# Performance work log

Measured on AMD Instinct MI355X. Metric: run time of the kernel, lower is better.

## Reference

```python
import jax, jax.numpy as jnp
import numpy as np

D_MODEL = 1024
D_STATE = 16
D_CONV = 4
EXPAND = 2
D_INNER = EXPAND * D_MODEL           # 2048
DT_RANK = (D_MODEL + 15) // 16       # 64
BATCH = 2
SEQ = 1024


def setup_inputs() -> dict:
    key = jax.random.key(0)
    ks = jax.random.split(key, 8)
    s = 0.02
    x = jax.random.normal(ks[0], (BATCH, SEQ, D_MODEL), jnp.float32)
    in_proj_w = jax.random.normal(ks[1], (2 * D_INNER, D_MODEL), jnp.float32) * s
    conv_w = jax.random.normal(ks[2], (D_INNER, 1, D_CONV), jnp.float32) * s
    conv_b = jnp.zeros((D_INNER,), jnp.float32)
    x_proj_w = jax.random.normal(ks[3], (DT_RANK + 2 * D_STATE, D_INNER), jnp.float32) * s
    dt_proj_w = jax.random.normal(ks[4], (D_INNER, DT_RANK), jnp.float32) * s
    # bias init so softplus(dt) lands in a sane small-dt range
    dt_proj_b = jnp.full((D_INNER,), -4.0, jnp.float32) + 0.1 * jax.random.normal(ks[5], (D_INNER,), jnp.float32)
    # standard S4D-real init: A = -[1..d_state], stored as log
    A_log = jnp.log(jnp.broadcast_to(jnp.arange(1, D_STATE + 1, dtype=jnp.float32), (D_INNER, D_STATE)))
    D_param = jnp.ones((D_INNER,), jnp.float32)
    out_proj_w = jax.random.normal(ks[6], (D_MODEL, D_INNER), jnp.float32) * s
    ln_w = jnp.ones((D_MODEL,), jnp.float32)
    ln_b = jnp.zeros((D_MODEL,), jnp.float32)
    return dict(x=x, in_proj_w=in_proj_w, conv_w=conv_w, conv_b=conv_b,
                x_proj_w=x_proj_w, dt_proj_w=dt_proj_w, dt_proj_b=dt_proj_b,
                A_log=A_log, D_param=D_param, out_proj_w=out_proj_w,
                ln_w=ln_w, ln_b=ln_b)


def _vim_block(x, in_proj_w, conv_w, conv_b, x_proj_w, dt_proj_w, dt_proj_b,
               A_log, D_param, out_proj_w, ln_w, ln_b):
    B, L, Dm = x.shape
    # in_proj (no bias) -> split into conv branch and gate z
    xz = jnp.einsum('bld,ed->ble', x, in_proj_w)          # (B,L,2*d_inner)
    xc, z = jnp.split(xz, 2, axis=-1)
    # causal depthwise conv1d over time
    xc_ncl = jnp.transpose(xc, (0, 2, 1))                  # (B,d_inner,L)
    conv = jax.lax.conv_general_dilated(
        xc_ncl, conv_w, window_strides=(1,), padding=[(D_CONV - 1, 0)],
        dimension_numbers=('NCH', 'OIH', 'NCH'), feature_group_count=D_INNER)
    conv = conv + conv_b[None, :, None]
    u = jax.nn.silu(jnp.transpose(conv, (0, 2, 1)))        # (B,L,d_inner)
    # input-dependent dt, B, C
    x_dbl = jnp.einsum('bld,ed->ble', u, x_proj_w)         # (B,L,dt_rank+2N)
    dt, Bmat, Cmat = jnp.split(x_dbl, [DT_RANK, DT_RANK + D_STATE], axis=-1)
    delta = jax.nn.softplus(jnp.einsum('blr,dr->bld', dt, dt_proj_w) + dt_proj_b)  # (B,L,d_inner)
    A = -jnp.exp(A_log)                                    # (d_inner,N)
    # discretize: ZOH for A, Euler for B (as in mamba selective_scan)
    deltaA = jnp.exp(delta[..., None] * A)                 # (B,L,d_inner,N)
    deltaBu = (delta * u)[..., None] * Bmat[:, :, None, :] # (B,L,d_inner,N)

    def step(h, inp):
        dA_t, dBu_t, C_t = inp                             # (B,d,N),(B,d,N),(B,N)
        h = dA_t * h + dBu_t
        y_t = jnp.einsum('bdn,bn->bd', h, C_t)
        return h, y_t

    h0 = jnp.zeros((B, D_INNER, D_STATE), x.dtype)
    xs = (jnp.moveaxis(deltaA, 1, 0), jnp.moveaxis(deltaBu, 1, 0), jnp.moveaxis(Cmat, 1, 0))
    _, ys = jax.lax.scan(step, h0, xs)                     # ys: (L,B,d_inner)
    y = jnp.moveaxis(ys, 0, 1) + u * D_param               # (B,L,d_inner)
    y = y * jax.nn.silu(z)                                 # gate
    out = jnp.einsum('bld,ed->ble', y, out_proj_w)         # (B,L,D)
    # residual + LayerNorm
    r = x + out
    mu = jnp.mean(r, axis=-1, keepdims=True)
    var = jnp.mean(jnp.square(r - mu), axis=-1, keepdims=True)
    return (r - mu) * jax.lax.rsqrt(var + 1e-5) * ln_w + ln_b


def reference(x, in_proj_w, conv_w, conv_b, x_proj_w, dt_proj_w, dt_proj_b,
              A_log, D_param, out_proj_w, ln_w, ln_b):
    return _vim_block(x, in_proj_w, conv_w, conv_b, x_proj_w, dt_proj_w, dt_proj_b,
                      A_log, D_param, out_proj_w, ln_w, ln_b)
```

## Files before the change

kernel.cpp:

```cpp
#include <hip/hip_runtime.h>
#include <math.h>

#define D_MODEL 1024
#define D_STATE 16
#define D_INNER 2048
#define DT_RANK 64
#define BATCH 2
#define SEQ 1024
#define NTOK (BATCH*SEQ)
#define NC 32
#define TC 32

typedef __attribute__((ext_vector_type(8))) short short8;
typedef __attribute__((ext_vector_type(4))) float f32x4;

__device__ __forceinline__ float siluf(float x){ return x / (1.0f + __expf(-x)); }
__device__ __forceinline__ float softplusf(float x){ return x > 20.f ? x : log1pf(__expf(x)); }

__device__ __forceinline__ unsigned short f2bf(float f){
    unsigned int x = __float_as_uint(f);
    unsigned int r = (x + 0x7FFFu + ((x >> 16) & 1u)) >> 16;
    return (unsigned short)r;
}
__device__ __forceinline__ float bf2f(unsigned short u){
    return __uint_as_float(((unsigned int)u) << 16);
}

__device__ __forceinline__ void gl_lds16(const unsigned short* g, unsigned short* l)
{
    __builtin_amdgcn_global_load_lds(
        (const __attribute__((address_space(1))) unsigned int*)g,
        (__attribute__((address_space(3))) unsigned int*)l, 16, 0, 0);
}

#define CR0 524288
#define CR1 1572864
#define CR2 1622016
#define CR3 1654784
#define CR4 2179072
__global__ __launch_bounds__(256)
void cvt_all(const float* __restrict__ s0, const float* __restrict__ s1,
             const float* __restrict__ s2, const float* __restrict__ s3,
             const float* __restrict__ s4,
             unsigned short* __restrict__ d0, unsigned short* __restrict__ d1,
             unsigned short* __restrict__ d2, unsigned short* __restrict__ d3,
             unsigned short* __restrict__ d4)
{
    int i = blockIdx.x * 256 + threadIdx.x;
    const float* s; unsigned short* dd; int base;
    if      (i < CR0) { s = s0; dd = d0; base = 0;   }
    else if (i < CR1) { s = s1; dd = d1; base = CR0; }
    else if (i < CR2) { s = s2; dd = d2; base = CR1; }
    else if (i < CR3) { s = s3; dd = d3; base = CR2; }
    else              { s = s4; dd = d4; base = CR3; }
    int j = (i - base) * 4;
    float4 v = *reinterpret_cast<const float4*>(&s[j]);
    ushort4 o;
    o.x = f2bf(v.x); o.y = f2bf(v.y); o.z = f2bf(v.z); o.w = f2bf(v.w);
    *reinterpret_cast<ushort4*>(&dd[j]) = o;
}

template<int EPI, int OB, int NVALID>
__global__ __launch_bounds__(256)
void gemm128(const unsigned short* __restrict__ A, int lda,
             const unsigned short* __restrict__ W, int ldw,
             const float* __restrict__ bias,
             void* __restrict__ Cv, int ldc,
             int M, int K)
{
    __shared__ __align__(16) unsigned short As[2][128 * 32];
    __shared__ __align__(16) unsigned short Ws[2][128 * 32];
    float* Cf = (float*)Cv;
    unsigned short* Cb = (unsigned short*)Cv;
    const int tid = threadIdx.x;

    const int nwg = gridDim.x * gridDim.y;
    int orig = blockIdx.y * gridDim.x + blockIdx.x;
    const int q = nwg >> 3, r = nwg & 7;
    int xcd = orig & 7, sub = orig >> 3;
    int wg = (xcd < r ? xcd * (q + 1) : r * (q + 1) + (xcd - r) * q) + sub;
    const int m0 = (wg / gridDim.x) * 128;
    const int n0 = (wg % gridDim.x) * 128;

    const size_t kbase = (size_t)blockIdx.z * K;
    const size_t zoff = (size_t)blockIdx.z * M * ldc;
    Cf += zoff; Cb += zoff;

    const int wave = tid >> 6, lane = tid & 63;
    const int wr = wave >> 1, wc = wave & 1;
    const int lr = lane & 15, lg = lane >> 4;

    const int gr = lane >> 2;
    const int gc = (lane & 3) * 8;
    const unsigned short* Ab = A + kbase + gc + (size_t)(m0 + wave * 32 + gr) * lda;
    const unsigned short* Wb = W + kbase + gc + (size_t)(n0 + wave * 32 + gr) * ldw;
    const int lo = (wave * 32) * 32;

    f32x4 acc[4][4];
#pragma unroll
    for (int i = 0; i < 4; i++)
#pragma unroll
        for (int j = 0; j < 4; j++) acc[i][j] = (f32x4)0.f;

    auto STAGE = [&](int buf, int kk) {
        gl_lds16(Ab + kk,            &As[buf][lo]);
        gl_lds16(Ab + kk + 16 * lda, &As[buf][lo + 16 * 32]);
        gl_lds16(Wb + kk,            &Ws[buf][lo]);
        gl_lds16(Wb + kk + 16 * ldw, &Ws[buf][lo + 16 * 32]);
    };
    auto COMPUTE = [&](int buf) {
        short8 af[4], bfr[4];
#pragma unroll
        for (int i = 0; i < 4; i++)
            af[i] = *reinterpret_cast<const short8*>(&As[buf][(wr * 64 + i * 16 + lr) * 32 + lg * 8]);
#pragma unroll
        for (int j = 0; j < 4; j++)
            bfr[j] = *reinterpret_cast<const short8*>(&Ws[buf][(wc * 64 + j * 16 + lr) * 32 + lg * 8]);
#pragma unroll
        for (int i = 0; i < 4; i++)
#pragma unroll
            for (int j = 0; j < 4; j++)
                acc[i][j] = __builtin_amdgcn_mfma_f32_16x16x32_bf16(af[i], bfr[j], acc[i][j], 0, 0, 0);
    };

    STAGE(0, 0);
    __syncthreads();
    for (int k0 = 0; k0 < K; k0 += 64) {
        if (k0 + 32 < K) STAGE(1, k0 + 32);
        COMPUTE(0);
        __syncthreads();
        if (k0 + 64 < K) STAGE(0, k0 + 64);
        COMPUTE(1);
        __syncthreads();
    }

#pragma unroll
    for (int i = 0; i < 4; i++) {
#pragma unroll
        for (int j = 0; j < 4; j++) {
            int col = n0 + wc * 64 + j * 16 + lr;
            if (NVALID > 0 && col >= NVALID) continue;
            int rbase = m0 + wr * 64 + i * 16 + lg * 4;
#pragma unroll
            for (int q2 = 0; q2 < 4; q2++) {
                float v = acc[i][j][q2];
                if (EPI == 1) v = softplusf(v + bias[col]);
                if (OB) Cb[(size_t)(rbase + q2) * ldc + col] = f2bf(v);
                else    Cf[(size_t)(rbase + q2) * ldc + col] = v;
            }
        }
    }
}

__global__ __launch_bounds__(256)
void conv_silu(const unsigned short* __restrict__ xz, const float* __restrict__ cw,
               const float* __restrict__ cb, unsigned short* __restrict__ u)
{
    int idx = blockIdx.x * 256 + threadIdx.x;
    int c = idx & (D_INNER - 1);
    int l = (idx >> 11) & (SEQ - 1);
    int b = idx >> 21;
    float4 w = *reinterpret_cast<const float4*>(&cw[c * 4]);
    float wk[4] = {w.x, w.y, w.z, w.w};
    float acc = cb[c];
    const unsigned short* xp = xz + (size_t)b * SEQ * (2 * D_INNER) + c;
#pragma unroll
    for (int k = 0; k < 4; k++) {
        int lk = l - 3 + k;
        if (lk >= 0) acc = fmaf(wk[k], bf2f(xp[(size_t)lk * (2 * D_INNER)]), acc);
    }
    u[idx] = f2bf(siluf(acc));
}

__global__ __launch_bounds__(256)
void reduce_xproj(const float* __restrict__ part, float* __restrict__ xdbl,
                  unsigned short* __restrict__ dt_bf)
{
    int idx = blockIdx.x * 256 + threadIdx.x;
    float s = 0.f;
#pragma unroll
    for (int z = 0; z < 8; z++) s += part[(size_t)z * NTOK * 96 + idx];
    xdbl[idx] = s;
    int c = idx % 96, m = idx / 96;
    if (c < DT_RANK) dt_bf[m * DT_RANK + c] = f2bf(s);
}

__global__ __launch_bounds__(256)
void scan_phase1(const unsigned short* __restrict__ delta, const unsigned short* __restrict__ u,
                 const float* __restrict__ xdbl,  const float* __restrict__ A_log,
                 float* __restrict__ P, float* __restrict__ Q)
{
    __shared__ float sB[TC][16];
    const int tid = threadIdx.x;
    const int dblk = blockIdx.x & 7;
    const int cc = (blockIdx.x >> 3) & (NC - 1);
    const int b  = blockIdx.x >> 8;
    const int d  = dblk * 256 + tid;
    const int t0 = cc * TC;

    float A[16];
#pragma unroll
    for (int i = 0; i < 4; i++) {
        float4 al = *reinterpret_cast<const float4*>(&A_log[d * 16 + i * 4]);
        A[i*4+0] = -__expf(al.x); A[i*4+1] = -__expf(al.y);
        A[i*4+2] = -__expf(al.z); A[i*4+3] = -__expf(al.w);
    }
    for (int e = tid; e < TC * 16; e += 256) {
        int t = e >> 4, j = e & 15;
        sB[t][j] = xdbl[((size_t)b * SEQ + t0 + t) * 96 + DT_RANK + j];
    }
    __syncthreads();

    float h[16];
#pragma unroll
    for (int n = 0; n < 16; n++) h[n] = 0.f;
    float sum = 0.f;
#pragma unroll 4
    for (int t = 0; t < TC; t++) {
        size_t tok = (size_t)b * SEQ + t0 + t;
        float dv = bf2f(delta[tok * D_INNER + d]);
        float uv = bf2f(u[tok * D_INNER + d]);
        sum += dv;
        float du = dv * uv;
#pragma unroll
        for (int n = 0; n < 16; n++)
            h[n] = fmaf(__expf(dv * A[n]), h[n], du * sB[t][n]);
    }
    size_t off = ((size_t)(cc * BATCH + b) * D_INNER + d) * 16;
#pragma unroll
    for (int i = 0; i < 4; i++) {
        float4 pv = make_float4(__expf(A[i*4+0]*sum), __expf(A[i*4+1]*sum),
                                __expf(A[i*4+2]*sum), __expf(A[i*4+3]*sum));
        *reinterpret_cast<float4*>(&P[off + i*4]) = pv;
        *reinterpret_cast<float4*>(&Q[off + i*4]) =
            make_float4(h[i*4+0], h[i*4+1], h[i*4+2], h[i*4+3]);
    }
}

__global__ __launch_bounds__(256)
void scan_phase2(const float* __restrict__ P, float* __restrict__ Q)
{
    int idx = blockIdx.x * 256 + threadIdx.x;
    int b = idx >> 15, rem = idx & 32767;
    float h = 0.f;
#pragma unroll
    for (int cc = 0; cc < NC; cc++) {
        size_t off = (size_t)(cc * BATCH + b) * (D_INNER * D_STATE) + rem;
        float p = P[off], q = Q[off];
        Q[off] = h;
        h = fmaf(p, h, q);
    }
}

__global__ __launch_bounds__(256)
void scan_phase3(const unsigned short* __restrict__ delta, const unsigned short* __restrict__ u,
                 const unsigned short* __restrict__ xz, const float* __restrict__ xdbl,
                 const float* __restrict__ A_log, const float* __restrict__ Dp,
                 const float* __restrict__ Hin,   unsigned short* __restrict__ yg)
{
    __shared__ float sB[TC][16], sC[TC][16];
    const int tid = threadIdx.x;
    const int dblk = blockIdx.x & 7;
    const int cc = (blockIdx.x >> 3) & (NC - 1);
    const int b  = blockIdx.x >> 8;
    const int d  = dblk * 256 + tid;
    const int t0 = cc * TC;

    float A[16];
#pragma unroll
    for (int i = 0; i < 4; i++) {
        float4 al = *reinterpret_cast<const float4*>(&A_log[d * 16 + i * 4]);
        A[i*4+0] = -__expf(al.x); A[i*4+1] = -__expf(al.y);
        A[i*4+2] = -__expf(al.z); A[i*4+3] = -__expf(al.w);
    }
    const float Dcoef = Dp[d];
    for (int e = tid; e < TC * 16; e += 256) {
        int t = e >> 4, j = e & 15;
        size_t tok = (size_t)b * SEQ + t0 + t;
        sB[t][j] = xdbl[tok * 96 + DT_RANK + j];
        sC[t][j] = xdbl[tok * 96 + DT_RANK + D_STATE + j];
    }
    float h[16];
    {
        size_t off = ((size_t)(cc * BATCH + b) * D_INNER + d) * 16;
#pragma unroll
        for (int i = 0; i < 4; i++) {
            float4 hv = *reinterpret_cast<const float4*>(&Hin[off + i*4]);
            h[i*4+0] = hv.x; h[i*4+1] = hv.y; h[i*4+2] = hv.z; h[i*4+3] = hv.w;
        }
    }
    __syncthreads();

#pragma unroll 4
    for (int t = 0; t < TC; t++) {
        size_t tok = (size_t)b * SEQ + t0 + t;
        float dv = bf2f(delta[tok * D_INNER + d]);
        float uv = bf2f(u[tok * D_INNER + d]);
        float zv = bf2f(xz[tok * (2 * D_INNER) + D_INNER + d]);
        float du = dv * uv;
        float y = 0.f;
#pragma unroll
        for (int n = 0; n < 16; n++) {
            h[n] = fmaf(__expf(dv * A[n]), h[n], du * sB[t][n]);
            y = fmaf(h[n], sC[t][n], y);
        }
        y += uv * Dcoef;
        yg[tok * D_INNER + d] = f2bf(y * siluf(zv));
    }
}

__global__ __launch_bounds__(256)
void ln4_kernel(const float* __restrict__ x, const unsigned short* __restrict__ p,
                const float* __restrict__ w, const float* __restrict__ bsc,
                float* __restrict__ out)
{
    __shared__ float red[2][4];
    const int t = blockIdx.x;
    const size_t base = (size_t)t * D_MODEL;
    const size_t S = (size_t)NTOK * D_MODEL;
    const int tid = threadIdx.x;
    const int c0 = tid * 4;
    float4 xv = *reinterpret_cast<const float4*>(&x[base + c0]);
    ushort4 p0 = *reinterpret_cast<const ushort4*>(&p[base + c0]);
    ushort4 p1 = *reinterpret_cast<const ushort4*>(&p[S + base + c0]);
    ushort4 p2 = *reinterpret_cast<const ushort4*>(&p[2 * S + base + c0]);
    ushort4 p3 = *reinterpret_cast<const ushort4*>(&p[3 * S + base + c0]);
    float v[4];
    v[0] = xv.x + bf2f(p0.x) + bf2f(p1.x) + bf2f(p2.x) + bf2f(p3.x);
    v[1] = xv.y + bf2f(p0.y) + bf2f(p1.y) + bf2f(p2.y) + bf2f(p3.y);
    v[2] = xv.z + bf2f(p0.z) + bf2f(p1.z) + bf2f(p2.z) + bf2f(p3.z);
    v[3] = xv.w + bf2f(p0.w) + bf2f(p1.w) + bf2f(p2.w) + bf2f(p3.w);
    float s = 0.f, s2 = 0.f;
#pragma unroll
    for (int i = 0; i < 4; i++) { s += v[i]; s2 = fmaf(v[i], v[i], s2); }
#pragma unroll
    for (int off = 32; off >= 1; off >>= 1) {
        s  += __shfl_down(s,  off);
        s2 += __shfl_down(s2, off);
    }
    int lane = tid & 63, wid = tid >> 6;
    if (lane == 0) { red[0][wid] = s; red[1][wid] = s2; }
    __syncthreads();
    float S1 = red[0][0] + red[0][1] + red[0][2] + red[0][3];
    float S2 = red[1][0] + red[1][1] + red[1][2] + red[1][3];
    float mu  = S1 * (1.f / D_MODEL);
    float var = S2 * (1.f / D_MODEL) - mu * mu;
    float rstd = rsqrtf(var + 1e-5f);
    float4 wv = *reinterpret_cast<const float4*>(&w[c0]);
    float4 bv = *reinterpret_cast<const float4*>(&bsc[c0]);
    float4 ov;
    ov.x = (v[0] - mu) * rstd * wv.x + bv.x;
    ov.y = (v[1] - mu) * rstd * wv.y + bv.y;
    ov.z = (v[2] - mu) * rstd * wv.z + bv.z;
    ov.w = (v[3] - mu) * rstd * wv.w + bv.w;
    *reinterpret_cast<float4*>(&out[base + c0]) = ov;
}

extern "C" void kernel_launch(void* const* d_in, const int* in_sizes, int n_in,
                              void* d_out, int out_size, void* d_ws, size_t ws_size,
                              hipStream_t stream)
{
    const float* x         = (const float*)d_in[0];
    const float* in_proj_w = (const float*)d_in[1];
    const float* conv_w    = (const float*)d_in[2];
    const float* conv_b    = (const float*)d_in[3];
    const float* x_proj_w  = (const float*)d_in[4];
    const float* dt_proj_w = (const float*)d_in[5];
    const float* dt_proj_b = (const float*)d_in[6];
    const float* A_log     = (const float*)d_in[7];
    const float* D_param   = (const float*)d_in[8];
    const float* out_proj_w= (const float*)d_in[9];
    const float* ln_w      = (const float*)d_in[10];
    const float* ln_b      = (const float*)d_in[11];
    float* out = (float*)d_out;

    unsigned short* xzb = (unsigned short*)d_ws;
    float* xdbl     = (float*)(xzb + (size_t)NTOK * 4096);
    float* partials = xdbl + (size_t)NTOK * 96;
    unsigned short* dlb = (unsigned short*)(partials + (size_t)8 * NTOK * 96);
    unsigned short* ub  = dlb + (size_t)NTOK * D_INNER;
    unsigned short* ygb = ub  + (size_t)NTOK * D_INNER;
    unsigned short* xb  = ygb + (size_t)NTOK * D_INNER;
    unsigned short* wib = xb  + (size_t)NTOK * D_MODEL;
    unsigned short* wxb = wib + (size_t)4096 * 1024;
    unsigned short* wdb = wxb + (size_t)96 * 2048;
    unsigned short* wob = wdb + (size_t)2048 * 64;
    unsigned short* dtb = wob + (size_t)1024 * 2048;
    float* Pbuf = (float*)(dtb + (size_t)NTOK * 64);
    float* Qbuf = Pbuf + (size_t)NC * BATCH * D_INNER * D_STATE;
    unsigned short* opart = xzb;

    dim3 blk(256);

    cvt_all<<<dim3(CR4 / 256), blk, 0, stream>>>(
        x, in_proj_w, x_proj_w, dt_proj_w, out_proj_w,
        xb, wib, wxb, wdb, wob);

    gemm128<0, 1, 0><<<dim3(4096 / 128, NTOK / 128, 1), blk, 0, stream>>>(
        xb, D_MODEL, wib, D_MODEL, nullptr, xzb, 2 * D_INNER, NTOK, D_MODEL);

    conv_silu<<<dim3((NTOK * D_INNER) / 256), blk, 0, stream>>>(xzb, conv_w, conv_b, ub);

    gemm128<0, 0, 96><<<dim3(1, NTOK / 128, 8), blk, 0, stream>>>(
        ub, D_INNER, wxb, D_INNER, nullptr, partials, 96, NTOK, 2048 / 8);

    reduce_xproj<<<dim3((NTOK * 96) / 256), blk, 0, stream>>>(partials, xdbl, dtb);

    gemm128<1, 1, 0><<<dim3(D_INNER / 128, NTOK / 128, 1), blk, 0, stream>>>(
        dtb, DT_RANK, wdb, DT_RANK, dt_proj_b, dlb, D_INNER, NTOK, DT_RANK);

    scan_phase1<<<dim3(BATCH * NC * (D_INNER / 256)), blk, 0, stream>>>(
        dlb, ub, xdbl, A_log, Pbuf, Qbuf);
    scan_phase2<<<dim3((BATCH * D_INNER * D_STATE) / 256), blk, 0, stream>>>(Pbuf, Qbuf);
    scan_phase3<<<dim3(BATCH * NC * (D_INNER / 256)), blk, 0, stream>>>(
        dlb, ub, xzb, xdbl, A_log, D_param, Qbuf, ygb);

    gemm128<0, 1, 0><<<dim3(D_MODEL / 128, NTOK / 128, 4), blk, 0, stream>>>(
        ygb, D_INNER, wob, D_INNER, nullptr, opart, D_MODEL, NTOK, D_INNER / 4);

    ln4_kernel<<<dim3(NTOK), blk, 0, stream>>>(x, opart, ln_w, ln_b, out);
}
```

Measured before the change: 173.1 us.

## Increase split-K across all GEMMs and vectorize conv with summed partials

The in_proj GEMM is split-K by 2, x_proj by 16 and out_proj by 8, so each launch has more blocks to fill the GPU. The conv and scan_phase3 consumers now sum the two in_proj bf16 partials on read, and the LayerNorm kernel sums eight out_proj partials. The conv kernel is vectorized to process four channels per thread, and the workspace layout is reshuffled to alias P/Q onto the x buffer. The cost is extra partial-buffer memory traffic and extra bf16 rounding error from summing partials.

Result: slower. 187.2 us (+8.2%).

```diff
diff --git a/kernel.cpp b/kernel.cpp
--- a/kernel.cpp
+++ b/kernel.cpp
@@ -153,23 +153,44 @@
 }
 
 __global__ __launch_bounds__(256)
-void conv_silu(const unsigned short* __restrict__ xz, const float* __restrict__ cw,
-               const float* __restrict__ cb, unsigned short* __restrict__ u)
-{
+void conv_silu4(const unsigned short* __restrict__ xzp, const float* __restrict__ cw,
+                const float* __restrict__ cb, unsigned short* __restrict__ u)
+{
+    const size_t PS = (size_t)NTOK * 4096;
     int idx = blockIdx.x * 256 + threadIdx.x;
-    int c = idx & (D_INNER - 1);
-    int l = (idx >> 11) & (SEQ - 1);
-    int b = idx >> 21;
-    float4 w = *reinterpret_cast<const float4*>(&cw[c * 4]);
-    float wk[4] = {w.x, w.y, w.z, w.w};
-    float acc = cb[c];
-    const unsigned short* xp = xz + (size_t)b * SEQ * (2 * D_INNER) + c;
+    int cq  = idx & 511;
+    int c0  = cq * 4;
+    int tok = idx >> 9;
+    int l   = tok & (SEQ - 1);
+
+    float4 w0 = *reinterpret_cast<const float4*>(&cw[(c0 + 0) * 4]);
+    float4 w1 = *reinterpret_cast<const float4*>(&cw[(c0 + 1) * 4]);
+    float4 w2 = *reinterpret_cast<const float4*>(&cw[(c0 + 2) * 4]);
+    float4 w3 = *reinterpret_cast<const float4*>(&cw[(c0 + 3) * 4]);
+    float4 bv = *reinterpret_cast<const float4*>(&cb[c0]);
+    float acc0 = bv.x, acc1 = bv.y, acc2 = bv.z, acc3 = bv.w;
+
 #pragma unroll
     for (int k = 0; k < 4; k++) {
         int lk = l - 3 + k;
-        if (lk >= 0) acc = fmaf(wk[k], bf2f(xp[(size_t)lk * (2 * D_INNER)]), acc);
-    }
-    u[idx] = f2bf(siluf(acc));
+        if (lk >= 0) {
+            size_t base = (size_t)(tok - 3 + k) * 4096 + c0;
+            ushort4 a = *reinterpret_cast<const ushort4*>(&xzp[base]);
+            ushort4 b = *reinterpret_cast<const ushort4*>(&xzp[PS + base]);
+            float x0 = bf2f(a.x) + bf2f(b.x);
+            float x1 = bf2f(a.y) + bf2f(b.y);
+            float x2 = bf2f(a.z) + bf2f(b.z);
+            float x3 = bf2f(a.w) + bf2f(b.w);
+            acc0 = fmaf(((const float*)&w0)[k], x0, acc0);
+            acc1 = fmaf(((const float*)&w1)[k], x1, acc1);
+            acc2 = fmaf(((const float*)&w2)[k], x2, acc2);
+            acc3 = fmaf(((const float*)&w3)[k], x3, acc3);
+        }
+    }
+    ushort4 o;
+    o.x = f2bf(siluf(acc0)); o.y = f2bf(siluf(acc1));
+    o.z = f2bf(siluf(acc2)); o.w = f2bf(siluf(acc3));
+    *reinterpret_cast<ushort4*>(&u[(size_t)tok * D_INNER + c0]) = o;
 }
 
 __global__ __launch_bounds__(256)
@@ -179,7 +200,7 @@
     int idx = blockIdx.x * 256 + threadIdx.x;
     float s = 0.f;
 #pragma unroll
-    for (int z = 0; z < 8; z++) s += part[(size_t)z * NTOK * 96 + idx];
+    for (int z = 0; z < 16; z++) s += part[(size_t)z * NTOK * 96 + idx];
     xdbl[idx] = s;
     int c = idx % 96, m = idx / 96;
     if (c < DT_RANK) dt_bf[m * DT_RANK + c] = f2bf(s);
@@ -254,11 +275,12 @@
 
 __global__ __launch_bounds__(256)
 void scan_phase3(const unsigned short* __restrict__ delta, const unsigned short* __restrict__ u,
-                 const unsigned short* __restrict__ xz, const float* __restrict__ xdbl,
+                 const unsigned short* __restrict__ xzp, const float* __restrict__ xdbl,
                  const float* __restrict__ A_log, const float* __restrict__ Dp,
                  const float* __restrict__ Hin,   unsigned short* __restrict__ yg)
 {
     __shared__ float sB[TC][16], sC[TC][16];
+    const size_t PS = (size_t)NTOK * 4096;
     const int tid = threadIdx.x;
     const int dblk = blockIdx.x & 7;
     const int cc = (blockIdx.x >> 3) & (NC - 1);
@@ -296,7 +318,8 @@
         size_t tok = (size_t)b * SEQ + t0 + t;
         float dv = bf2f(delta[tok * D_INNER + d]);
         float uv = bf2f(u[tok * D_INNER + d]);
-        float zv = bf2f(xz[tok * (2 * D_INNER) + D_INNER + d]);
+        size_t zi = tok * 4096 + D_INNER + d;
+        float zv = bf2f(xzp[zi]) + bf2f(xzp[PS + zi]);
         float du = dv * uv;
         float y = 0.f;
 #pragma unroll
@@ -310,7 +333,7 @@
 }
 
 __global__ __launch_bounds__(256)
-void ln4_kernel(const float* __restrict__ x, const unsigned short* __restrict__ p,
+void ln8_kernel(const float* __restrict__ x, const unsigned short* __restrict__ p,
                 const float* __restrict__ w, const float* __restrict__ bsc,
                 float* __restrict__ out)
 {
@@ -321,15 +344,13 @@
     const int tid = threadIdx.x;
     const int c0 = tid * 4;
     float4 xv = *reinterpret_cast<const float4*>(&x[base + c0]);
-    ushort4 p0 = *reinterpret_cast<const ushort4*>(&p[base + c0]);
-    ushort4 p1 = *reinterpret_cast<const ushort4*>(&p[S + base + c0]);
-    ushort4 p2 = *reinterpret_cast<const ushort4*>(&p[2 * S + base + c0]);
-    ushort4 p3 = *reinterpret_cast<const ushort4*>(&p[3 * S + base + c0]);
-    float v[4];
-    v[0] = xv.x + bf2f(p0.x) + bf2f(p1.x) + bf2f(p2.x) + bf2f(p3.x);
-    v[1] = xv.y + bf2f(p0.y) + bf2f(p1.y) + bf2f(p2.y) + bf2f(p3.y);
-    v[2] = xv.z + bf2f(p0.z) + bf2f(p1.z) + bf2f(p2.z) + bf2f(p3.z);
-    v[3] = xv.w + bf2f(p0.w) + bf2f(p1.w) + bf2f(p2.w) + bf2f(p3.w);
+    float v[4] = {xv.x, xv.y, xv.z, xv.w};
+#pragma unroll
+    for (int z = 0; z < 8; z++) {
+        ushort4 pv = *reinterpret_cast<const ushort4*>(&p[z * S + base + c0]);
+        v[0] += bf2f(pv.x); v[1] += bf2f(pv.y);
+        v[2] += bf2f(pv.z); v[3] += bf2f(pv.w);
+    }
     float s = 0.f, s2 = 0.f;
 #pragma unroll
     for (int i = 0; i < 4; i++) { s += v[i]; s2 = fmaf(v[i], v[i], s2); }
@@ -374,21 +395,21 @@
     const float* ln_b      = (const float*)d_in[11];
     float* out = (float*)d_out;
 
-    unsigned short* xzb = (unsigned short*)d_ws;
-    float* xdbl     = (float*)(xzb + (size_t)NTOK * 4096);
-    float* partials = xdbl + (size_t)NTOK * 96;
-    unsigned short* dlb = (unsigned short*)(partials + (size_t)8 * NTOK * 96);
+    unsigned short* xzp = (unsigned short*)d_ws;
+    float* xdbl = (float*)(xzp + (size_t)2 * NTOK * 4096);
+    unsigned short* dlb = (unsigned short*)(xdbl + (size_t)NTOK * 96);
     unsigned short* ub  = dlb + (size_t)NTOK * D_INNER;
     unsigned short* ygb = ub  + (size_t)NTOK * D_INNER;
     unsigned short* xb  = ygb + (size_t)NTOK * D_INNER;
     unsigned short* wib = xb  + (size_t)NTOK * D_MODEL;
     unsigned short* wxb = wib + (size_t)4096 * 1024;
     unsigned short* wdb = wxb + (size_t)96 * 2048;
-    unsigned short* wob = wdb + (size_t)2048 * 64;
-    unsigned short* dtb = wob + (size_t)1024 * 2048;
-    float* Pbuf = (float*)(dtb + (size_t)NTOK * 64);
+    unsigned short* dtb = wdb + (size_t)2048 * 64;
+    float* xpart = (float*)(dtb + (size_t)NTOK * 64);
+    float* Pbuf = (float*)xb;
     float* Qbuf = Pbuf + (size_t)NC * BATCH * D_INNER * D_STATE;
-    unsigned short* opart = xzb;
+    unsigned short* wob = (unsigned short*)(xpart + (size_t)16 * NTOK * 96);
+    unsigned short* opart = xzp;
 
     dim3 blk(256);
 
@@ -396,15 +417,15 @@
         x, in_proj_w, x_proj_w, dt_proj_w, out_proj_w,
         xb, wib, wxb, wdb, wob);
 
-    gemm128<0, 1, 0><<<dim3(4096 / 128, NTOK / 128, 1), blk, 0, stream>>>(
-        xb, D_MODEL, wib, D_MODEL, nullptr, xzb, 2 * D_INNER, NTOK, D_MODEL);
-
-    conv_silu<<<dim3((NTOK * D_INNER) / 256), blk, 0, stream>>>(xzb, conv_w, conv_b, ub);
-
-    gemm128<0, 0, 96><<<dim3(1, NTOK / 128, 8), blk, 0, stream>>>(
-        ub, D_INNER, wxb, D_INNER, nullptr, partials, 96, NTOK, 2048 / 8);
-
-    reduce_xproj<<<dim3((NTOK * 96) / 256), blk, 0, stream>>>(partials, xdbl, dtb);
+    gemm128<0, 1, 0><<<dim3(4096 / 128, NTOK / 128, 2), blk, 0, stream>>>(
+        xb, D_MODEL, wib, D_MODEL, nullptr, xzp, 2 * D_INNER, NTOK, D_MODEL / 2);
+
+    conv_silu4<<<dim3((NTOK * 512) / 256), blk, 0, stream>>>(xzp, conv_w, conv_b, ub);
+
+    gemm128<0, 0, 96><<<dim3(1, NTOK / 128, 16), blk, 0, stream>>>(
+        ub, D_INNER, wxb, D_INNER, nullptr, xpart, 96, NTOK, 2048 / 16);
+
+    reduce_xproj<<<dim3((NTOK * 96) / 256), blk, 0, stream>>>(xpart, xdbl, dtb);
 
     gemm128<1, 1, 0><<<dim3(D_INNER / 128, NTOK / 128, 1), blk, 0, stream>>>(
         dtb, DT_RANK, wdb, DT_RANK, dt_proj_b, dlb, D_INNER, NTOK, DT_RANK);
@@ -413,10 +434,10 @@
         dlb, ub, xdbl, A_log, Pbuf, Qbuf);
     scan_phase2<<<dim3((BATCH * D_INNER * D_STATE) / 256), blk, 0, stream>>>(Pbuf, Qbuf);
     scan_phase3<<<dim3(BATCH * NC * (D_INNER / 256)), blk, 0, stream>>>(
-        dlb, ub, xzb, xdbl, A_log, D_param, Qbuf, ygb);
-
-    gemm128<0, 1, 0><<<dim3(D_MODEL / 128, NTOK / 128, 4), blk, 0, stream>>>(
-        ygb, D_INNER, wob, D_INNER, nullptr, opart, D_MODEL, NTOK, D_INNER / 4);
-
-    ln4_kernel<<<dim3(NTOK), blk, 0, stream>>>(x, opart, ln_w, ln_b, out);
-}
+        dlb, ub, xzp, xdbl, A_log, D_param, Qbuf, ygb);
+
+    gemm128<0, 1, 0><<<dim3(D_MODEL / 128, NTOK / 128, 8), blk, 0, stream>>>(
+        ygb, D_INNER, wob, D_INNER, nullptr, opart, D_MODEL, NTOK, D_INNER / 8);
+
+    ln8_kernel<<<dim3(NTOK), blk, 0, stream>>>(x, opart, ln_w, ln_b, out);
+}
```

## Fuse three scan phases into one cooperative kernel and vectorize conv

Applied to the files above, without the earlier changes.

The three chunked-scan kernels become one cooperative kernel that uses grid-wide syncs between the chunk-local scan, the cross-chunk carry propagation and the output pass. This removes two kernel launches and their tail gaps. The depthwise conv kernel now handles four channels per thread with ushort4 loads and stores instead of one scalar element per thread. The cooperative launch requires all 512 blocks to be resident at once, and the grid syncs add barrier cost.

After: 326.0 us. 88.3% more time.

```diff
diff --git a/kernel.cpp b/kernel.cpp
--- a/kernel.cpp
+++ b/kernel.cpp
@@ -1,5 +1,8 @@
 #include <hip/hip_runtime.h>
+#include <hip/hip_cooperative_groups.h>
 #include <math.h>
+
+namespace cg = cooperative_groups;
 
 #define D_MODEL 1024
 #define D_STATE 16
@@ -153,23 +156,38 @@
 }
 
 __global__ __launch_bounds__(256)
-void conv_silu(const unsigned short* __restrict__ xz, const float* __restrict__ cw,
-               const float* __restrict__ cb, unsigned short* __restrict__ u)
+void conv_silu4(const unsigned short* __restrict__ xz, const float* __restrict__ cw,
+                const float* __restrict__ cb, unsigned short* __restrict__ u)
 {
     int idx = blockIdx.x * 256 + threadIdx.x;
-    int c = idx & (D_INNER - 1);
-    int l = (idx >> 11) & (SEQ - 1);
-    int b = idx >> 21;
-    float4 w = *reinterpret_cast<const float4*>(&cw[c * 4]);
-    float wk[4] = {w.x, w.y, w.z, w.w};
-    float acc = cb[c];
-    const unsigned short* xp = xz + (size_t)b * SEQ * (2 * D_INNER) + c;
+    int cq  = idx & 511;
+    int c0  = cq * 4;
+    int tok = idx >> 9;
+    int l   = tok & (SEQ - 1);
+
+    float4 w0 = *reinterpret_cast<const float4*>(&cw[(c0 + 0) * 4]);
+    float4 w1 = *reinterpret_cast<const float4*>(&cw[(c0 + 1) * 4]);
+    float4 w2 = *reinterpret_cast<const float4*>(&cw[(c0 + 2) * 4]);
+    float4 w3 = *reinterpret_cast<const float4*>(&cw[(c0 + 3) * 4]);
+    float4 bv = *reinterpret_cast<const float4*>(&cb[c0]);
+    float acc0 = bv.x, acc1 = bv.y, acc2 = bv.z, acc3 = bv.w;
+
 #pragma unroll
     for (int k = 0; k < 4; k++) {
         int lk = l - 3 + k;
-        if (lk >= 0) acc = fmaf(wk[k], bf2f(xp[(size_t)lk * (2 * D_INNER)]), acc);
-    }
-    u[idx] = f2bf(siluf(acc));
+        if (lk >= 0) {
+            size_t base = (size_t)(tok - 3 + k) * 4096 + c0;
+            ushort4 a = *reinterpret_cast<const ushort4*>(&xz[base]);
+            acc0 = fmaf(((const float*)&w0)[k], bf2f(a.x), acc0);
+            acc1 = fmaf(((const float*)&w1)[k], bf2f(a.y), acc1);
+            acc2 = fmaf(((const float*)&w2)[k], bf2f(a.z), acc2);
+            acc3 = fmaf(((const float*)&w3)[k], bf2f(a.w), acc3);
+        }
+    }
+    ushort4 o;
+    o.x = f2bf(siluf(acc0)); o.y = f2bf(siluf(acc1));
+    o.z = f2bf(siluf(acc2)); o.w = f2bf(siluf(acc3));
+    *reinterpret_cast<ushort4*>(&u[(size_t)tok * D_INNER + c0]) = o;
 }
 
 __global__ __launch_bounds__(256)
@@ -186,78 +204,13 @@
 }
 
 __global__ __launch_bounds__(256)
-void scan_phase1(const unsigned short* __restrict__ delta, const unsigned short* __restrict__ u,
-                 const float* __restrict__ xdbl,  const float* __restrict__ A_log,
-                 float* __restrict__ P, float* __restrict__ Q)
-{
-    __shared__ float sB[TC][16];
-    const int tid = threadIdx.x;
-    const int dblk = blockIdx.x & 7;
-    const int cc = (blockIdx.x >> 3) & (NC - 1);
-    const int b  = blockIdx.x >> 8;
-    const int d  = dblk * 256 + tid;
-    const int t0 = cc * TC;
-
-    float A[16];
-#pragma unroll
-    for (int i = 0; i < 4; i++) {
-        float4 al = *reinterpret_cast<const float4*>(&A_log[d * 16 + i * 4]);
-        A[i*4+0] = -__expf(al.x); A[i*4+1] = -__expf(al.y);
-        A[i*4+2] = -__expf(al.z); A[i*4+3] = -__expf(al.w);
-    }
-    for (int e = tid; e < TC * 16; e += 256) {
-        int t = e >> 4, j = e & 15;
-        sB[t][j] = xdbl[((size_t)b * SEQ + t0 + t) * 96 + DT_RANK + j];
-    }
-    __syncthreads();
-
-    float h[16];
-#pragma unroll
-    for (int n = 0; n < 16; n++) h[n] = 0.f;
-    float sum = 0.f;
-#pragma unroll 4
-    for (int t = 0; t < TC; t++) {
-        size_t tok = (size_t)b * SEQ + t0 + t;
-        float dv = bf2f(delta[tok * D_INNER + d]);
-        float uv = bf2f(u[tok * D_INNER + d]);
-        sum += dv;
-        float du = dv * uv;
-#pragma unroll
-        for (int n = 0; n < 16; n++)
-            h[n] = fmaf(__expf(dv * A[n]), h[n], du * sB[t][n]);
-    }
-    size_t off = ((size_t)(cc * BATCH + b) * D_INNER + d) * 16;
-#pragma unroll
-    for (int i = 0; i < 4; i++) {
-        float4 pv = make_float4(__expf(A[i*4+0]*sum), __expf(A[i*4+1]*sum),
-                                __expf(A[i*4+2]*sum), __expf(A[i*4+3]*sum));
-        *reinterpret_cast<float4*>(&P[off + i*4]) = pv;
-        *reinterpret_cast<float4*>(&Q[off + i*4]) =
-            make_float4(h[i*4+0], h[i*4+1], h[i*4+2], h[i*4+3]);
-    }
-}
-
-__global__ __launch_bounds__(256)
-void scan_phase2(const float* __restrict__ P, float* __restrict__ Q)
-{
-    int idx = blockIdx.x * 256 + threadIdx.x;
-    int b = idx >> 15, rem = idx & 32767;
-    float h = 0.f;
-#pragma unroll
-    for (int cc = 0; cc < NC; cc++) {
-        size_t off = (size_t)(cc * BATCH + b) * (D_INNER * D_STATE) + rem;
-        float p = P[off], q = Q[off];
-        Q[off] = h;
-        h = fmaf(p, h, q);
-    }
-}
-
-__global__ __launch_bounds__(256)
-void scan_phase3(const unsigned short* __restrict__ delta, const unsigned short* __restrict__ u,
-                 const unsigned short* __restrict__ xz, const float* __restrict__ xdbl,
-                 const float* __restrict__ A_log, const float* __restrict__ Dp,
-                 const float* __restrict__ Hin,   unsigned short* __restrict__ yg)
-{
+void scan_fused(const unsigned short* __restrict__ delta, const unsigned short* __restrict__ u,
+                const unsigned short* __restrict__ xz,    const float* __restrict__ xdbl,
+                const float* __restrict__ A_log, const float* __restrict__ Dp,
+                float* __restrict__ P, float* __restrict__ Q,
+                unsigned short* __restrict__ yg)
+{
+    cg::grid_group grid = cg::this_grid();
     __shared__ float sB[TC][16], sC[TC][16];
     const int tid = threadIdx.x;
     const int dblk = blockIdx.x & 7;
@@ -280,32 +233,76 @@
         sB[t][j] = xdbl[tok * 96 + DT_RANK + j];
         sC[t][j] = xdbl[tok * 96 + DT_RANK + D_STATE + j];
     }
-    float h[16];
+    __syncthreads();
+
+    const size_t off = ((size_t)(cc * BATCH + b) * D_INNER + d) * 16;
+
     {
-        size_t off = ((size_t)(cc * BATCH + b) * D_INNER + d) * 16;
+        float h[16];
+#pragma unroll
+        for (int n = 0; n < 16; n++) h[n] = 0.f;
+        float sum = 0.f;
+#pragma unroll 4
+        for (int t = 0; t < TC; t++) {
+            size_t tok = (size_t)b * SEQ + t0 + t;
+            float dv = bf2f(delta[tok * D_INNER + d]);
+            float uv = bf2f(u[tok * D_INNER + d]);
+            sum += dv;
+            float du = dv * uv;
+#pragma unroll
+            for (int n = 0; n < 16; n++)
+                h[n] = fmaf(__expf(dv * A[n]), h[n], du * sB[t][n]);
+        }
 #pragma unroll
         for (int i = 0; i < 4; i++) {
-            float4 hv = *reinterpret_cast<const float4*>(&Hin[off + i*4]);
+            float4 pv = make_float4(__expf(A[i*4+0]*sum), __expf(A[i*4+1]*sum),
+                                    __expf(A[i*4+2]*sum), __expf(A[i*4+3]*sum));
+            *reinterpret_cast<float4*>(&P[off + i*4]) = pv;
+            *reinterpret_cast<float4*>(&Q[off + i*4]) =
+                make_float4(h[i*4+0], h[i*4+1], h[i*4+2], h[i*4+3]);
+        }
+    }
+    grid.sync();
+
+    {
+        int idx = blockIdx.x * 256 + tid;
+        if (idx < BATCH * D_INNER * D_STATE) {
+            int bb = idx >> 15, rem = idx & 32767;
+            float h = 0.f;
+#pragma unroll
+            for (int c2 = 0; c2 < NC; c2++) {
+                size_t o2 = (size_t)(c2 * BATCH + bb) * (D_INNER * D_STATE) + rem;
+                float p = P[o2], qv = Q[o2];
+                Q[o2] = h;
+                h = fmaf(p, h, qv);
+            }
+        }
+    }
+    grid.sync();
+
+    {
+        float h[16];
+#pragma unroll
+        for (int i = 0; i < 4; i++) {
+            float4 hv = *reinterpret_cast<const float4*>(&Q[off + i*4]);
             h[i*4+0] = hv.x; h[i*4+1] = hv.y; h[i*4+2] = hv.z; h[i*4+3] = hv.w;
         }
-    }
-    __syncthreads();
-
 #pragma unroll 4
-    for (int t = 0; t < TC; t++) {
-        size_t tok = (size_t)b * SEQ + t0 + t;
-        float dv = bf2f(delta[tok * D_INNER + d]);
-        float uv = bf2f(u[tok * D_INNER + d]);
-        float zv = bf2f(xz[tok * (2 * D_INNER) + D_INNER + d]);
-        float du = dv * uv;
-        float y = 0.f;
-#pragma unroll
-        for (int n = 0; n < 16; n++) {
-            h[n] = fmaf(__expf(dv * A[n]), h[n], du * sB[t][n]);
-            y = fmaf(h[n], sC[t][n], y);
-        }
-        y += uv * Dcoef;
-        yg[tok * D_INNER + d] = f2bf(y * siluf(zv));
+        for (int t = 0; t < TC; t++) {
+            size_t tok = (size_t)b * SEQ + t0 + t;
+            float dv = bf2f(delta[tok * D_INNER + d]);
+            float uv = bf2f(u[tok * D_INNER + d]);
+            float zv = bf2f(xz[tok * (2 * D_INNER) + D_INNER + d]);
+            float du = dv * uv;
+            float y = 0.f;
+#pragma unroll
+            for (int n = 0; n < 16; n++) {
+                h[n] = fmaf(__expf(dv * A[n]), h[n], du * sB[t][n]);
+                y = fmaf(h[n], sC[t][n], y);
+            }
+            y += uv * Dcoef;
+            yg[tok * D_INNER + d] = f2bf(y * siluf(zv));
+        }
     }
 }
 
@@ -399,7 +396,7 @@
     gemm128<0, 1, 0><<<dim3(4096 / 128, NTOK / 128, 1), blk, 0, stream>>>(
         xb, D_MODEL, wib, D_MODEL, nullptr, xzb, 2 * D_INNER, NTOK, D_MODEL);
 
-    conv_silu<<<dim3((NTOK * D_INNER) / 256), blk, 0, stream>>>(xzb, conv_w, conv_b, ub);
+    conv_silu4<<<dim3((NTOK * 512) / 256), blk, 0, stream>>>(xzb, conv_w, conv_b, ub);
 
     gemm128<0, 0, 96><<<dim3(1, NTOK / 128, 8), blk, 0, stream>>>(
         ub, D_INNER, wxb, D_INNER, nullptr, partials, 96, NTOK, 2048 / 8);
@@ -409,11 +406,16 @@
     gemm128<1, 1, 0><<<dim3(D_INNER / 128, NTOK / 128, 1), blk, 0, stream>>>(
         dtb, DT_RANK, wdb, DT_RANK, dt_proj_b, dlb, D_INNER, NTOK, DT_RANK);
 
-    scan_phase1<<<dim3(BATCH * NC * (D_INNER / 256)), blk, 0, stream>>>(
-        dlb, ub, xdbl, A_log, Pbuf, Qbuf);
-    scan_phase2<<<dim3((BATCH * D_INNER * D_STATE) / 256), blk, 0, stream>>>(Pbuf, Qbuf);
-    scan_phase3<<<dim3(BATCH * NC * (D_INNER / 256)), blk, 0, stream>>>(
-        dlb, ub, xzb, xdbl, A_log, D_param, Qbuf, ygb);
+    {
+        const unsigned short* a0 = dlb;  const unsigned short* a1 = ub;
+        const unsigned short* a2 = xzb;  const float* a3 = xdbl;
+        const float* a4 = A_log;         const float* a5 = D_param;
+        float* a6 = Pbuf;                float* a7 = Qbuf;
+        unsigned short* a8 = ygb;
+        void* sargs[] = {&a0, &a1, &a2, &a3, &a4, &a5, &a6, &a7, &a8};
+        hipLaunchCooperativeKernel((void*)scan_fused, dim3(BATCH * NC * (D_INNER / 256)),
+                                   blk, sargs, 0, stream);
+    }
 
     gemm128<0, 1, 0><<<dim3(D_MODEL / 128, NTOK / 128, 4), blk, 0, stream>>>(
         ygb, D_INNER, wob, D_INNER, nullptr, opart, D_MODEL, NTOK, D_INNER / 4);
```
